# Performance work log

Hardware: AMD Instinct MI355X
Metric: run time of the kernel (lower is better)

Reference implementation:

```python
import jax, jax.numpy as jnp
import numpy as np
from jax import lax

D_MODEL = 1024
D_STATE = 16
EXPAND = 2
KERNEL = 4
BATCH = 4
SEQ = 4096
LN_EPS = 1e-5


def _ln(x, w, b):
    m = jnp.mean(x, axis=-1, keepdims=True)
    v = jnp.mean((x - m) ** 2, axis=-1, keepdims=True)
    return (x - m) * lax.rsqrt(v + LN_EPS) * w + b


def setup_inputs() -> dict:
    key = jax.random.key(0)
    ks = jax.random.split(key, 16)
    d, n, e, k = D_MODEL, D_STATE, EXPAND, KERNEL

    def lin(key, fan_in, shape):
        bound = 1.0 / np.sqrt(fan_in)
        return jax.random.uniform(key, shape, jnp.float32, -bound, bound)

    return {
        "x": jax.random.normal(ks[0], (BATCH, SEQ, d), jnp.float32),
        "ln1_w": jnp.ones((d,), jnp.float32),
        "ln1_b": jnp.zeros((d,), jnp.float32),
        "conv_w": lin(ks[1], k, (d, 1, k)),  # depthwise conv, groups=d -> fan_in=k
        "conv_b": lin(ks[2], k, (d,)),
        "lns_w": jnp.ones((d,), jnp.float32),
        "lns_b": jnp.zeros((d,), jnp.float32),
        "in_w": lin(ks[3], d, (d, 2 * d)),
        "in_b": lin(ks[4], d, (2 * d,)),
        "xp_w": lin(ks[5], d, (d, n)),
        "xp_b": lin(ks[6], d, (n,)),
        "A_log": jax.random.normal(ks[7], (n,), jnp.float32),
        "D": jax.random.normal(ks[8], (n, d), jnp.float32),
        "out_w": lin(ks[9], d, (d, d)),
        "out_b": lin(ks[10], d, (d,)),
        "ln2_w": jnp.ones((d,), jnp.float32),
        "ln2_b": jnp.zeros((d,), jnp.float32),
        "mlp_w1": lin(ks[11], d, (d, e * d)),
        "mlp_b1": lin(ks[12], d, (e * d,)),
        "mlp_w2": lin(ks[13], e * d, (e * d, d)),
        "mlp_b2": lin(ks[14], e * d, (d,)),
    }


def reference(x, ln1_w, ln1_b, conv_w, conv_b, lns_w, lns_b, in_w, in_b,
              xp_w, xp_b, A_log, D, out_w, out_b, ln2_w, ln2_b,
              mlp_w1, mlp_b1, mlp_w2, mlp_b2):
    b, s, d = x.shape
    # --- depthwise causal-padded conv branch (truncated to seq_len) ---
    xn = _ln(x, ln1_w, ln1_b)
    xc = jnp.transpose(xn, (0, 2, 1))  # (b, d, s)
    xc = lax.conv_general_dilated(
        xc, conv_w, window_strides=(1,), padding=[(KERNEL - 1, KERNEL - 1)],
        feature_group_count=d, dimension_numbers=("NCH", "OIH", "NCH"))
    xc = xc + conv_b[None, :, None]
    xc = jnp.transpose(xc, (0, 2, 1))[:, :s]  # (b, s, d)
    x = x + xc

    # --- SelectiveScanLayer ---
    residual = x
    xn = _ln(x, lns_w, lns_b)
    xz = xn @ in_w + in_b
    xp, z = jnp.split(xz, 2, axis=-1)
    xp = jax.nn.silu(xp)
    z = jax.nn.sigmoid(z)
    u = xp @ xp_w + xp_b  # (b, s, n)
    decay = jnp.exp(-jnp.exp(A_log))  # exp(A), A = -exp(A_log); (n,)

    u_t = jnp.transpose(u, (1, 0, 2))  # (s, b, n)

    def step(h, u_i):
        h = decay * h + u_i
        return h, h

    _, hs = lax.scan(step, jnp.zeros((b, D_STATE), x.dtype), u_t)  # (s, b, n)
    ys = jnp.einsum("sbn,nd->sbd", hs, D) * jnp.transpose(z, (1, 0, 2))
    ys = ys @ out_w + out_b  # (s, b, d)
    # faithful to original: torch stack gives (1,s,b,d), then .view(b,s,d)
    y = ys.reshape(b, s, d)
    x = residual + y

    # --- MLP (dropout inactive at eval) ---
    h = _ln(x, ln2_w, ln2_b)
    h = jax.nn.gelu(h @ mlp_w1 + mlp_b1, approximate=False)
    h = h @ mlp_w2 + mlp_b2
    return x + h
```

## Files before the change

kernel.cpp:

```cpp
#include <hip/hip_runtime.h>
#include <cstdint>
#include <cstddef>


typedef short bf16x8 __attribute__((ext_vector_type(8)));
typedef float f32x4 __attribute__((ext_vector_type(4)));

#define GLD16(gp, lp)                                                          \
  __builtin_amdgcn_global_load_lds(                                            \
      (__attribute__((address_space(1))) void*)(gp),                           \
      (__attribute__((address_space(3))) void*)(lp), 16, 0, 0)

static __device__ __forceinline__ ushort f2bf(float f) {
  union { float f; uint32_t u; } c; c.f = f;
  uint32_t r = c.u + 0x7FFFu + ((c.u >> 16) & 1u);
  return (ushort)(r >> 16);
}
static __device__ __forceinline__ float bf2f(ushort u) {
  union { uint32_t u; float f; } c; c.u = ((uint32_t)u) << 16;
  return c.f;
}

template <int BF16OUT>
__global__ __launch_bounds__(256) void ln_kernel(
    const float* __restrict__ x, const float* __restrict__ w,
    const float* __restrict__ b, void* __restrict__ out) {
  const int row = blockIdx.x;
  const int tid = threadIdx.x;
  const float4 v = ((const float4*)(x + (size_t)row * 1024))[tid];
  float s  = v.x + v.y + v.z + v.w;
  float s2 = v.x * v.x + v.y * v.y + v.z * v.z + v.w * v.w;
#pragma unroll
  for (int off = 32; off > 0; off >>= 1) {
    s  += __shfl_down(s, off);
    s2 += __shfl_down(s2, off);
  }
  __shared__ float red[8];
  const int wv = tid >> 6, ln = tid & 63;
  if (ln == 0) { red[wv] = s; red[4 + wv] = s2; }
  __syncthreads();
  s  = red[0] + red[1] + red[2] + red[3];
  s2 = red[4] + red[5] + red[6] + red[7];
  const float mean = s * (1.f / 1024.f);
  const float var  = s2 * (1.f / 1024.f) - mean * mean;
  const float rstd = rsqrtf(var + 1e-5f);
  const float4 wv4 = ((const float4*)w)[tid];
  const float4 bv4 = ((const float4*)b)[tid];
  const float o0 = (v.x - mean) * rstd * wv4.x + bv4.x;
  const float o1 = (v.y - mean) * rstd * wv4.y + bv4.y;
  const float o2 = (v.z - mean) * rstd * wv4.z + bv4.z;
  const float o3 = (v.w - mean) * rstd * wv4.w + bv4.w;
  if (BF16OUT) {
    ushort4 o; o.x = f2bf(o0); o.y = f2bf(o1); o.z = f2bf(o2); o.w = f2bf(o3);
    ((ushort4*)((ushort*)out + (size_t)row * 1024))[tid] = o;
  } else {
    float4 o; o.x = o0; o.y = o1; o.z = o2; o.w = o3;
    ((float4*)((float*)out + (size_t)row * 1024))[tid] = o;
  }
}

__global__ __launch_bounds__(256) void conv_kernel(
    const float* __restrict__ x, const float* __restrict__ xn,
    const float* __restrict__ cw, const float* __restrict__ cb,
    float* __restrict__ x1) {
  const size_t i = (size_t)blockIdx.x * 256 + threadIdx.x;
  const int c4 = (int)(i & 255);
  const size_t row = i >> 8;
  const int t = (int)(row & 4095);
  const int c0 = c4 * 4;
  float4 acc = *(const float4*)(cb + c0);
  const float4 w0 = *(const float4*)(cw + (size_t)(c0 + 0) * 4);
  const float4 w1 = *(const float4*)(cw + (size_t)(c0 + 1) * 4);
  const float4 w2 = *(const float4*)(cw + (size_t)(c0 + 2) * 4);
  const float4 w3 = *(const float4*)(cw + (size_t)(c0 + 3) * 4);
  const float4* xnb = (const float4*)xn;
  const size_t rowbase = (row - (size_t)t) << 8;
#pragma unroll
  for (int j = 0; j < 4; j++) {
    const int tt = t - 3 + j;
    if (tt >= 0) {
      const float4 xv = xnb[rowbase + (size_t)tt * 256 + c4];
      acc.x += xv.x * ((const float*)&w0)[j];
      acc.y += xv.y * ((const float*)&w1)[j];
      acc.z += xv.z * ((const float*)&w2)[j];
      acc.w += xv.w * ((const float*)&w3)[j];
    }
  }
  const float4 xv0 = ((const float4*)x)[i];
  float4 o;
  o.x = xv0.x + acc.x; o.y = xv0.y + acc.y;
  o.z = xv0.z + acc.z; o.w = xv0.w + acc.w;
  ((float4*)x1)[i] = o;
}

__global__ __launch_bounds__(256) void wt_kernel(
    const float* __restrict__ w, ushort* __restrict__ wt, int K, int N) {
  __shared__ float tile[32][33];
  const int tx = threadIdx.x & 31, ty = threadIdx.x >> 5;
  const int n0 = blockIdx.x * 32, k0 = blockIdx.y * 32;
#pragma unroll
  for (int j = 0; j < 32; j += 8)
    tile[ty + j][tx] = w[(size_t)(k0 + ty + j) * N + n0 + tx];
  __syncthreads();
#pragma unroll
  for (int j = 0; j < 32; j += 8)
    wt[(size_t)(n0 + ty + j) * K + k0 + tx] = f2bf(tile[tx][ty + j]);
}

__global__ __launch_bounds__(256) void u_kernel(
    const ushort* __restrict__ xp, const float* __restrict__ w,
    const float* __restrict__ wb, float* __restrict__ u) {
  const int tid = threadIdx.x;
  const int r = tid >> 4, n = tid & 15;
  const size_t row = (size_t)blockIdx.x * 16 + r;
  const ushort* xr = xp + row * 1024;
  float acc = wb[n];
  for (int k = 0; k < 1024; k += 8) {
    const uint4 pk = *(const uint4*)(xr + k);
    const ushort* pp = (const ushort*)&pk;
#pragma unroll
    for (int j = 0; j < 8; j++)
      acc += bf2f(pp[j]) * w[(size_t)(k + j) * 16 + n];
  }
  u[row * 16 + n] = acc;
}

__global__ __launch_bounds__(256) void scan_kernel(
    const float* __restrict__ u, const float* __restrict__ A_log,
    float* __restrict__ hs) {
  const int tid = threadIdx.x;
  const int b = blockIdx.x >> 4;
  const int n = blockIdx.x & 15;
  const float d = expf(-expf(A_log[n]));
  const int t0 = tid * 16;
  const float* up = u + ((size_t)b * 4096) * 16 + n;
  float loc[16];
  float h = 0.f;
#pragma unroll
  for (int i = 0; i < 16; i++) {
    h = d * h + up[(size_t)(t0 + i) * 16];
    loc[i] = h;
  }
  __shared__ float sv[256];
  sv[tid] = h;
  __syncthreads();
  float d16 = d * d; d16 *= d16; d16 *= d16; d16 *= d16;
  float f = d16;
  for (int off = 1; off < 256; off <<= 1) {
    const float add = (tid >= off) ? sv[tid - off] : 0.f;
    __syncthreads();
    sv[tid] += f * add;
    __syncthreads();
    f *= f;
  }
  const float carry = (tid > 0) ? sv[tid - 1] : 0.f;
  float dp = d;
#pragma unroll
  for (int i = 0; i < 16; i++) {
    const float hg = loc[i] + dp * carry;
    dp *= d;
    hs[((size_t)(t0 + i) * 4 + b) * 16 + n] = hg;
  }
}

__global__ __launch_bounds__(256) void g_kernel(
    const float* __restrict__ hs, const float* __restrict__ Dm,
    const ushort* __restrict__ z, ushort* __restrict__ g) {
  __shared__ float hsh[256];
  const int tid = threadIdx.x;
  const int r0 = blockIdx.x * 16;
  hsh[tid] = hs[(size_t)r0 * 16 + tid];
  __syncthreads();
  float4 acc[16];
#pragma unroll
  for (int rr = 0; rr < 16; rr++) acc[rr] = make_float4(0.f, 0.f, 0.f, 0.f);
  const float4* Dv = (const float4*)Dm;
#pragma unroll
  for (int n = 0; n < 16; n++) {
    const float4 dv = Dv[(size_t)n * 256 + tid];
#pragma unroll
    for (int rr = 0; rr < 16; rr++) {
      const float h = hsh[rr * 16 + n];
      acc[rr].x += h * dv.x; acc[rr].y += h * dv.y;
      acc[rr].z += h * dv.z; acc[rr].w += h * dv.w;
    }
  }
#pragma unroll
  for (int rr = 0; rr < 16; rr++) {
    const int r = r0 + rr;
    const int b = r & 3, t = r >> 2;
    const ushort4 zv =
        *(const ushort4*)(z + ((size_t)b * 4096 + t) * 1024 + tid * 4);
    ushort4 o;
    o.x = f2bf(acc[rr].x * bf2f(zv.x)); o.y = f2bf(acc[rr].y * bf2f(zv.y));
    o.z = f2bf(acc[rr].z * bf2f(zv.z)); o.w = f2bf(acc[rr].w * bf2f(zv.w));
    *(ushort4*)(g + (size_t)r * 1024 + tid * 4) = o;
  }
}

template <int EPI>
__global__ __launch_bounds__(256) void gemm_bt(
    const ushort* __restrict__ A, const ushort* __restrict__ Bt,
    const float* __restrict__ bias, int K, void* __restrict__ p0,
    void* __restrict__ p1) {
  __shared__ ushort As[128 * 32];
  __shared__ ushort Bs[128 * 32];
  const int tid = threadIdx.x;
  const int wave = tid >> 6, lane = tid & 63;
  const int l16 = lane & 15, quad = lane >> 4;
  const int bm0 = blockIdx.y * 128, bn0 = blockIdx.x * 128;
  const int wr = (wave >> 1) * 64, wc = (wave & 1) * 64;
  const int srow = lane >> 2;
  const int skel = (((lane & 3) ^ ((srow >> 1) & 3)) << 3);

  const ushort* Ag = A + (size_t)(bm0 + wave * 32 + srow) * K + skel;
  const ushort* Bg = Bt + (size_t)(bn0 + wave * 32 + srow) * K + skel;
  ushort* Al = &As[wave * 32 * 32];
  ushort* Bl = &Bs[wave * 32 * 32];

  const int rswz = (l16 >> 1) & 3;
  const int coff = ((quad ^ rswz) << 3);

  f32x4 acc[4][4];
#pragma unroll
  for (int i = 0; i < 4; i++)
#pragma unroll
    for (int j = 0; j < 4; j++) acc[i][j] = (f32x4){0.f, 0.f, 0.f, 0.f};

  for (int k0 = 0; k0 < K; k0 += 32) {
    GLD16(Ag + k0, Al);
    GLD16(Ag + k0 + (size_t)16 * K, Al + 16 * 32);
    GLD16(Bg + k0, Bl);
    GLD16(Bg + k0 + (size_t)16 * K, Bl + 16 * 32);
    __syncthreads();
    bf16x8 aF[4], bF[4];
#pragma unroll
    for (int i = 0; i < 4; i++)
      aF[i] = *(const bf16x8*)&As[(wr + i * 16 + l16) * 32 + coff];
#pragma unroll
    for (int j = 0; j < 4; j++)
      bF[j] = *(const bf16x8*)&Bs[(wc + j * 16 + l16) * 32 + coff];
#pragma unroll
    for (int i = 0; i < 4; i++)
#pragma unroll
      for (int j = 0; j < 4; j++)
        acc[i][j] = __builtin_amdgcn_mfma_f32_16x16x32_bf16(
            aF[i], bF[j], acc[i][j], 0, 0, 0);
    __syncthreads();
  }

#pragma unroll
  for (int i = 0; i < 4; i++) {
    const int row0 = bm0 + wr + i * 16 + quad * 4;
#pragma unroll
    for (int j = 0; j < 4; j++) {
      const int c = bn0 + wc + j * 16 + l16;
      const float bv = bias[c];
#pragma unroll
      for (int r = 0; r < 4; r++) {
        const size_t row = (size_t)(row0 + r);
        const float v = acc[i][j][r] + bv;
        if (EPI == 0) {
          if (c < 1024)
            ((ushort*)p0)[row * 1024 + c] = f2bf(v / (1.f + __expf(-v)));
          else
            ((ushort*)p1)[row * 1024 + (c - 1024)] =
                f2bf(1.f / (1.f + __expf(-v)));
        } else if (EPI == 1) {
          float* io = (float*)p0;
          io[row * 1024 + c] += v;
        } else if (EPI == 2) {
          ((ushort*)p0)[row * 2048 + c] =
              f2bf(0.5f * v * (1.f + erff(v * 0.70710678118654752f)));
        } else {
          ((float*)p0)[row * 1024 + c] =
              ((const float*)p1)[row * 1024 + c] + v;
        }
      }
    }
  }
}

extern "C" void kernel_launch(void* const* d_in, const int* in_sizes, int n_in,
                              void* d_out, int out_size, void* d_ws,
                              size_t ws_size, hipStream_t stream) {
  const float* x      = (const float*)d_in[0];
  const float* ln1_w  = (const float*)d_in[1];
  const float* ln1_b  = (const float*)d_in[2];
  const float* conv_w = (const float*)d_in[3];
  const float* conv_b = (const float*)d_in[4];
  const float* lns_w  = (const float*)d_in[5];
  const float* lns_b  = (const float*)d_in[6];
  const float* in_w   = (const float*)d_in[7];
  const float* in_b   = (const float*)d_in[8];
  const float* xp_w   = (const float*)d_in[9];
  const float* xp_b   = (const float*)d_in[10];
  const float* A_log  = (const float*)d_in[11];
  const float* Dm     = (const float*)d_in[12];
  const float* out_w  = (const float*)d_in[13];
  const float* out_b  = (const float*)d_in[14];
  const float* ln2_w  = (const float*)d_in[15];
  const float* ln2_b  = (const float*)d_in[16];
  const float* mlp_w1 = (const float*)d_in[17];
  const float* mlp_b1 = (const float*)d_in[18];
  const float* mlp_w2 = (const float*)d_in[19];
  const float* mlp_b2 = (const float*)d_in[20];

  char* wsp = (char*)d_ws;
  size_t off = 0;
  auto alloc = [&](size_t bytes) {
    void* p = wsp + off;
    off += (bytes + 255) & ~(size_t)255;
    return p;
  };
  float*  x1    = (float*)alloc(67108864);
  float*  xn    = (float*)alloc(67108864);
  ushort* abuf  = (ushort*)xn;
  ushort* gbuf  = (ushort*)xn + 16777216;
  ushort* xpb   = (ushort*)alloc(33554432);
  ushort* zb    = (ushort*)alloc(67108864);
  ushort* h1b   = (ushort*)zb;
  float*  ub    = (float*)alloc(1048576);
  float*  hsb   = (float*)alloc(1048576);
  ushort* in_wT = (ushort*)alloc(4194304);
  ushort* out_wT= (ushort*)alloc(2097152);
  ushort* w1T   = (ushort*)alloc(4194304);
  ushort* w2T   = (ushort*)alloc(4194304);

  wt_kernel<<<dim3(64, 32), 256, 0, stream>>>(in_w, in_wT, 1024, 2048);
  wt_kernel<<<dim3(32, 32), 256, 0, stream>>>(out_w, out_wT, 1024, 1024);
  wt_kernel<<<dim3(64, 32), 256, 0, stream>>>(mlp_w1, w1T, 1024, 2048);
  wt_kernel<<<dim3(32, 64), 256, 0, stream>>>(mlp_w2, w2T, 2048, 1024);

  ln_kernel<0><<<16384, 256, 0, stream>>>(x, ln1_w, ln1_b, xn);
  conv_kernel<<<16384, 256, 0, stream>>>(x, xn, conv_w, conv_b, x1);
  ln_kernel<1><<<16384, 256, 0, stream>>>(x1, lns_w, lns_b, abuf);
  gemm_bt<0><<<dim3(16, 128), 256, 0, stream>>>(abuf, in_wT, in_b, 1024,
                                                xpb, zb);
  u_kernel<<<1024, 256, 0, stream>>>(xpb, xp_w, xp_b, ub);
  scan_kernel<<<64, 256, 0, stream>>>(ub, A_log, hsb);
  g_kernel<<<1024, 256, 0, stream>>>(hsb, Dm, zb, gbuf);
  gemm_bt<1><<<dim3(8, 128), 256, 0, stream>>>(gbuf, out_wT, out_b, 1024,
                                               x1, nullptr);
  ln_kernel<1><<<16384, 256, 0, stream>>>(x1, ln2_w, ln2_b, xpb);
  gemm_bt<2><<<dim3(16, 128), 256, 0, stream>>>(xpb, w1T, mlp_b1, 1024,
                                                h1b, nullptr);
  gemm_bt<3><<<dim3(8, 128), 256, 0, stream>>>(h1b, w2T, mlp_b2, 2048,
                                               d_out, x1);
}
```

Measured before the change: 767.2 us.

## Fuse LN+conv+LN, merge weight transposes, MFMA u-projection, deeper GEMM K-tile

Fuses the first layernorm, depthwise conv, residual add and second layernorm into one kernel that recomputes the LN of the 3 preceding rows instead of writing and rereading an fp32 normalized buffer. Merges the four weight-transpose launches into one. Replaces the scalar u projection with an MFMA kernel that stages bf16 weights in LDS. The main GEMM's K-step grows from 32 to 64 with a new XOR swizzle, and the grid swaps x/y so consecutive blocks walk M. These cut memory traffic and launch count, at the cost of redundant LN reductions in the fused kernel and more LDS per GEMM block.

```diff
diff --git a/kernel.cpp b/kernel.cpp
--- a/kernel.cpp
+++ b/kernel.cpp
@@ -59,70 +59,174 @@
   }
 }
 
-__global__ __launch_bounds__(256) void conv_kernel(
-    const float* __restrict__ x, const float* __restrict__ xn,
-    const float* __restrict__ cw, const float* __restrict__ cb,
-    float* __restrict__ x1) {
-  const size_t i = (size_t)blockIdx.x * 256 + threadIdx.x;
-  const int c4 = (int)(i & 255);
-  const size_t row = i >> 8;
-  const int t = (int)(row & 4095);
-  const int c0 = c4 * 4;
+__global__ __launch_bounds__(256) void lnconv_kernel(
+    const float* __restrict__ x, const float* __restrict__ ln1w,
+    const float* __restrict__ ln1b, const float* __restrict__ cw,
+    const float* __restrict__ cb, const float* __restrict__ lnsw,
+    const float* __restrict__ lnsb, float* __restrict__ x1,
+    ushort* __restrict__ abuf) {
+  const int row = blockIdx.x;
+  const int t = row & 4095;
+  const int tid = threadIdx.x;
+  const int wv = tid >> 6, ln = tid & 63;
+  const float4* x4 = (const float4*)x;
+  float4 xr[4];
+  float s[4], q[4];
+#pragma unroll
+  for (int j = 0; j < 4; j++) {
+    const int tt = t - 3 + j;
+    if (tt >= 0)
+      xr[j] = x4[(size_t)(row - 3 + j) * 256 + tid];
+    else
+      xr[j] = make_float4(0.f, 0.f, 0.f, 0.f);
+    s[j] = xr[j].x + xr[j].y + xr[j].z + xr[j].w;
+    q[j] = xr[j].x * xr[j].x + xr[j].y * xr[j].y + xr[j].z * xr[j].z +
+           xr[j].w * xr[j].w;
+  }
+#pragma unroll
+  for (int off = 32; off > 0; off >>= 1) {
+#pragma unroll
+    for (int j = 0; j < 4; j++) {
+      s[j] += __shfl_down(s[j], off);
+      q[j] += __shfl_down(q[j], off);
+    }
+  }
+  __shared__ float red[4][8];
+  __shared__ float red2[8];
+  if (ln == 0) {
+#pragma unroll
+    for (int j = 0; j < 4; j++) { red[wv][j] = s[j]; red[wv][4 + j] = q[j]; }
+  }
+  __syncthreads();
+  float4 wv4 = ((const float4*)ln1w)[tid];
+  float4 bv4 = ((const float4*)ln1b)[tid];
+  const int c0 = tid * 4;
   float4 acc = *(const float4*)(cb + c0);
   const float4 w0 = *(const float4*)(cw + (size_t)(c0 + 0) * 4);
   const float4 w1 = *(const float4*)(cw + (size_t)(c0 + 1) * 4);
   const float4 w2 = *(const float4*)(cw + (size_t)(c0 + 2) * 4);
   const float4 w3 = *(const float4*)(cw + (size_t)(c0 + 3) * 4);
-  const float4* xnb = (const float4*)xn;
-  const size_t rowbase = (row - (size_t)t) << 8;
 #pragma unroll
   for (int j = 0; j < 4; j++) {
-    const int tt = t - 3 + j;
-    if (tt >= 0) {
-      const float4 xv = xnb[rowbase + (size_t)tt * 256 + c4];
-      acc.x += xv.x * ((const float*)&w0)[j];
-      acc.y += xv.y * ((const float*)&w1)[j];
-      acc.z += xv.z * ((const float*)&w2)[j];
-      acc.w += xv.w * ((const float*)&w3)[j];
-    }
-  }
-  const float4 xv0 = ((const float4*)x)[i];
+    if (t - 3 + j >= 0) {
+      const float sm = red[0][j] + red[1][j] + red[2][j] + red[3][j];
+      const float sq = red[0][4 + j] + red[1][4 + j] + red[2][4 + j] +
+                       red[3][4 + j];
+      const float mean = sm * (1.f / 1024.f);
+      const float var  = sq * (1.f / 1024.f) - mean * mean;
+      const float rstd = rsqrtf(var + 1e-5f);
+      const float lx = (xr[j].x - mean) * rstd * wv4.x + bv4.x;
+      const float ly = (xr[j].y - mean) * rstd * wv4.y + bv4.y;
+      const float lz = (xr[j].z - mean) * rstd * wv4.z + bv4.z;
+      const float lw = (xr[j].w - mean) * rstd * wv4.w + bv4.w;
+      acc.x += lx * ((const float*)&w0)[j];
+      acc.y += ly * ((const float*)&w1)[j];
+      acc.z += lz * ((const float*)&w2)[j];
+      acc.w += lw * ((const float*)&w3)[j];
+    }
+  }
   float4 o;
-  o.x = xv0.x + acc.x; o.y = xv0.y + acc.y;
-  o.z = xv0.z + acc.z; o.w = xv0.w + acc.w;
-  ((float4*)x1)[i] = o;
-}
-
-__global__ __launch_bounds__(256) void wt_kernel(
-    const float* __restrict__ w, ushort* __restrict__ wt, int K, int N) {
+  o.x = xr[3].x + acc.x; o.y = xr[3].y + acc.y;
+  o.z = xr[3].z + acc.z; o.w = xr[3].w + acc.w;
+  ((float4*)x1)[(size_t)row * 256 + tid] = o;
+  float s2 = o.x + o.y + o.z + o.w;
+  float q2 = o.x * o.x + o.y * o.y + o.z * o.z + o.w * o.w;
+#pragma unroll
+  for (int off = 32; off > 0; off >>= 1) {
+    s2 += __shfl_down(s2, off);
+    q2 += __shfl_down(q2, off);
+  }
+  if (ln == 0) { red2[wv] = s2; red2[4 + wv] = q2; }
+  __syncthreads();
+  const float sm = red2[0] + red2[1] + red2[2] + red2[3];
+  const float sq = red2[4] + red2[5] + red2[6] + red2[7];
+  const float mean = sm * (1.f / 1024.f);
+  const float var  = sq * (1.f / 1024.f) - mean * mean;
+  const float rstd = rsqrtf(var + 1e-5f);
+  wv4 = ((const float4*)lnsw)[tid];
+  bv4 = ((const float4*)lnsb)[tid];
+  ushort4 a;
+  a.x = f2bf((o.x - mean) * rstd * wv4.x + bv4.x);
+  a.y = f2bf((o.y - mean) * rstd * wv4.y + bv4.y);
+  a.z = f2bf((o.z - mean) * rstd * wv4.z + bv4.z);
+  a.w = f2bf((o.w - mean) * rstd * wv4.w + bv4.w);
+  ((ushort4*)(abuf + (size_t)row * 1024))[tid] = a;
+}
+
+__global__ __launch_bounds__(256) void wt_all_kernel(
+    const float* __restrict__ in_w, const float* __restrict__ out_w,
+    const float* __restrict__ w1, const float* __restrict__ w2,
+    ushort* __restrict__ in_wT, ushort* __restrict__ out_wT,
+    ushort* __restrict__ w1T, ushort* __restrict__ w2T) {
   __shared__ float tile[32][33];
+  const int idx = blockIdx.x;
+  const float* src; ushort* dst; int K, N, n0, k0;
+  if (idx < 2048) {
+    src = in_w; dst = in_wT; K = 1024; N = 2048;
+    n0 = (idx & 63) * 32; k0 = (idx >> 6) * 32;
+  } else if (idx < 3072) {
+    const int r = idx - 2048;
+    src = out_w; dst = out_wT; K = 1024; N = 1024;
+    n0 = (r & 31) * 32; k0 = (r >> 5) * 32;
+  } else if (idx < 5120) {
+    const int r = idx - 3072;
+    src = w1; dst = w1T; K = 1024; N = 2048;
+    n0 = (r & 63) * 32; k0 = (r >> 6) * 32;
+  } else {
+    const int r = idx - 5120;
+    src = w2; dst = w2T; K = 2048; N = 1024;
+    n0 = (r & 31) * 32; k0 = (r >> 5) * 32;
+  }
   const int tx = threadIdx.x & 31, ty = threadIdx.x >> 5;
-  const int n0 = blockIdx.x * 32, k0 = blockIdx.y * 32;
 #pragma unroll
   for (int j = 0; j < 32; j += 8)
-    tile[ty + j][tx] = w[(size_t)(k0 + ty + j) * N + n0 + tx];
+    tile[ty + j][tx] = src[(size_t)(k0 + ty + j) * N + n0 + tx];
   __syncthreads();
 #pragma unroll
   for (int j = 0; j < 32; j += 8)
-    wt[(size_t)(n0 + ty + j) * K + k0 + tx] = f2bf(tile[tx][ty + j]);
-}
-
-__global__ __launch_bounds__(256) void u_kernel(
-    const ushort* __restrict__ xp, const float* __restrict__ w,
-    const float* __restrict__ wb, float* __restrict__ u) {
-  const int tid = threadIdx.x;
-  const int r = tid >> 4, n = tid & 15;
-  const size_t row = (size_t)blockIdx.x * 16 + r;
-  const ushort* xr = xp + row * 1024;
-  float acc = wb[n];
-  for (int k = 0; k < 1024; k += 8) {
-    const uint4 pk = *(const uint4*)(xr + k);
-    const ushort* pp = (const ushort*)&pk;
-#pragma unroll
-    for (int j = 0; j < 8; j++)
-      acc += bf2f(pp[j]) * w[(size_t)(k + j) * 16 + n];
-  }
-  u[row * 16 + n] = acc;
+    dst[(size_t)(n0 + ty + j) * K + k0 + tx] = f2bf(tile[tx][ty + j]);
+}
+
+__global__ __launch_bounds__(256) void u_mfma_kernel(
+    const ushort* __restrict__ xp, const float* __restrict__ xpw,
+    const float* __restrict__ xpb, float* __restrict__ u) {
+  __shared__ ushort Ws[16 * 1024];
+  __shared__ ushort As[64 * 64];
+  const int tid = threadIdx.x;
+  const int wave = tid >> 6, lane = tid & 63;
+  const int l16 = lane & 15, quad = lane >> 4;
+  for (int e = tid; e < 16384; e += 256) {
+    const int n = e & 15, k = e >> 4;
+    Ws[n * 1024 + (((k >> 3) ^ (n & 7)) << 3) + (k & 7)] =
+        f2bf(xpw[(size_t)k * 16 + n]);
+  }
+  const int bm0 = blockIdx.x * 64;
+  const int srow = lane >> 3, sblk = (lane & 7) ^ (srow & 7);
+  const ushort* Ag = xp + (size_t)(bm0 + wave * 16 + srow) * 1024 + sblk * 8;
+  ushort* Al = &As[wave * 16 * 64];
+  const int rsw = l16 & 7;
+  f32x4 acc = (f32x4){0.f, 0.f, 0.f, 0.f};
+  __syncthreads();
+  for (int k0 = 0; k0 < 1024; k0 += 64) {
+    GLD16(Ag + k0, Al);
+    GLD16(Ag + k0 + (size_t)8 * 1024, Al + 512);
+    __syncthreads();
+#pragma unroll
+    for (int kh = 0; kh < 2; kh++) {
+      const bf16x8 aF = *(const bf16x8*)
+          &As[(wave * 16 + l16) * 64 + (((kh * 4 + quad) ^ rsw) << 3)];
+      const bf16x8 bF = *(const bf16x8*)
+          &Ws[l16 * 1024 + ((((k0 >> 3) + kh * 4 + quad) ^ rsw) << 3)];
+      acc = __builtin_amdgcn_mfma_f32_16x16x32_bf16(aF, bF, acc, 0, 0, 0);
+    }
+    __syncthreads();
+  }
+  const float bv = xpb[l16];
+#pragma unroll
+  for (int r = 0; r < 4; r++) {
+    const int row = bm0 + wave * 16 + quad * 4 + r;
+    u[(size_t)row * 16 + l16] = acc[r] + bv;
+  }
 }
 
 __global__ __launch_bounds__(256) void scan_kernel(
@@ -203,23 +307,21 @@
     const ushort* __restrict__ A, const ushort* __restrict__ Bt,
     const float* __restrict__ bias, int K, void* __restrict__ p0,
     void* __restrict__ p1) {
-  __shared__ ushort As[128 * 32];
-  __shared__ ushort Bs[128 * 32];
+  __shared__ ushort As[128 * 64];
+  __shared__ ushort Bs[128 * 64];
   const int tid = threadIdx.x;
   const int wave = tid >> 6, lane = tid & 63;
   const int l16 = lane & 15, quad = lane >> 4;
-  const int bm0 = blockIdx.y * 128, bn0 = blockIdx.x * 128;
+  const int bm0 = blockIdx.x * 128, bn0 = blockIdx.y * 128;
   const int wr = (wave >> 1) * 64, wc = (wave & 1) * 64;
-  const int srow = lane >> 2;
-  const int skel = (((lane & 3) ^ ((srow >> 1) & 3)) << 3);
-
-  const ushort* Ag = A + (size_t)(bm0 + wave * 32 + srow) * K + skel;
-  const ushort* Bg = Bt + (size_t)(bn0 + wave * 32 + srow) * K + skel;
-  ushort* Al = &As[wave * 32 * 32];
-  ushort* Bl = &Bs[wave * 32 * 32];
-
-  const int rswz = (l16 >> 1) & 3;
-  const int coff = ((quad ^ rswz) << 3);
+  const int srow = lane >> 3;
+  const int sblk = (lane & 7) ^ (srow & 7);
+
+  const ushort* Ag = A + (size_t)(bm0 + wave * 32 + srow) * K + sblk * 8;
+  const ushort* Bg = Bt + (size_t)(bn0 + wave * 32 + srow) * K + sblk * 8;
+  ushort* Al = &As[wave * 32 * 64];
+  ushort* Bl = &Bs[wave * 32 * 64];
+  const int rsw = l16 & 7;
 
   f32x4 acc[4][4];
 #pragma unroll
@@ -227,25 +329,30 @@
 #pragma unroll
     for (int j = 0; j < 4; j++) acc[i][j] = (f32x4){0.f, 0.f, 0.f, 0.f};
 
-  for (int k0 = 0; k0 < K; k0 += 32) {
-    GLD16(Ag + k0, Al);
-    GLD16(Ag + k0 + (size_t)16 * K, Al + 16 * 32);
-    GLD16(Bg + k0, Bl);
-    GLD16(Bg + k0 + (size_t)16 * K, Bl + 16 * 32);
-    __syncthreads();
-    bf16x8 aF[4], bF[4];
-#pragma unroll
-    for (int i = 0; i < 4; i++)
-      aF[i] = *(const bf16x8*)&As[(wr + i * 16 + l16) * 32 + coff];
-#pragma unroll
-    for (int j = 0; j < 4; j++)
-      bF[j] = *(const bf16x8*)&Bs[(wc + j * 16 + l16) * 32 + coff];
-#pragma unroll
-    for (int i = 0; i < 4; i++)
+  for (int k0 = 0; k0 < K; k0 += 64) {
+#pragma unroll
+    for (int i = 0; i < 4; i++) {
+      GLD16(Ag + (size_t)(i * 8) * K + k0, Al + i * 512);
+      GLD16(Bg + (size_t)(i * 8) * K + k0, Bl + i * 512);
+    }
+    __syncthreads();
+#pragma unroll
+    for (int kh = 0; kh < 2; kh++) {
+      const int c8 = ((kh * 4 + quad) ^ rsw) << 3;
+      bf16x8 aF[4], bF[4];
+#pragma unroll
+      for (int i = 0; i < 4; i++)
+        aF[i] = *(const bf16x8*)&As[(wr + i * 16 + l16) * 64 + c8];
 #pragma unroll
       for (int j = 0; j < 4; j++)
-        acc[i][j] = __builtin_amdgcn_mfma_f32_16x16x32_bf16(
-            aF[i], bF[j], acc[i][j], 0, 0, 0);
+        bF[j] = *(const bf16x8*)&Bs[(wc + j * 16 + l16) * 64 + c8];
+#pragma unroll
+      for (int i = 0; i < 4; i++)
+#pragma unroll
+        for (int j = 0; j < 4; j++)
+          acc[i][j] = __builtin_amdgcn_mfma_f32_16x16x32_bf16(
+              aF[i], bF[j], acc[i][j], 0, 0, 0);
+    }
     __syncthreads();
   }
 
@@ -314,9 +421,8 @@
     return p;
   };
   float*  x1    = (float*)alloc(67108864);
-  float*  xn    = (float*)alloc(67108864);
-  ushort* abuf  = (ushort*)xn;
-  ushort* gbuf  = (ushort*)xn + 16777216;
+  ushort* abuf  = (ushort*)alloc(67108864);
+  ushort* gbuf  = abuf + 16777216;
   ushort* xpb   = (ushort*)alloc(33554432);
   ushort* zb    = (ushort*)alloc(67108864);
   ushort* h1b   = (ushort*)zb;
@@ -327,24 +433,20 @@
   ushort* w1T   = (ushort*)alloc(4194304);
   ushort* w2T   = (ushort*)alloc(4194304);
 
-  wt_kernel<<<dim3(64, 32), 256, 0, stream>>>(in_w, in_wT, 1024, 2048);
-  wt_kernel<<<dim3(32, 32), 256, 0, stream>>>(out_w, out_wT, 1024, 1024);
-  wt_kernel<<<dim3(64, 32), 256, 0, stream>>>(mlp_w1, w1T, 1024, 2048);
-  wt_kernel<<<dim3(32, 64), 256, 0, stream>>>(mlp_w2, w2T, 2048, 1024);
-
-  ln_kernel<0><<<16384, 256, 0, stream>>>(x, ln1_w, ln1_b, xn);
-  conv_kernel<<<16384, 256, 0, stream>>>(x, xn, conv_w, conv_b, x1);
-  ln_kernel<1><<<16384, 256, 0, stream>>>(x1, lns_w, lns_b, abuf);
-  gemm_bt<0><<<dim3(16, 128), 256, 0, stream>>>(abuf, in_wT, in_b, 1024,
+  wt_all_kernel<<<7168, 256, 0, stream>>>(in_w, out_w, mlp_w1, mlp_w2,
+                                          in_wT, out_wT, w1T, w2T);
+  lnconv_kernel<<<16384, 256, 0, stream>>>(x, ln1_w, ln1_b, conv_w, conv_b,
+                                           lns_w, lns_b, x1, abuf);
+  gemm_bt<0><<<dim3(128, 16), 256, 0, stream>>>(abuf, in_wT, in_b, 1024,
                                                 xpb, zb);
-  u_kernel<<<1024, 256, 0, stream>>>(xpb, xp_w, xp_b, ub);
+  u_mfma_kernel<<<256, 256, 0, stream>>>(xpb, xp_w, xp_b, ub);
   scan_kernel<<<64, 256, 0, stream>>>(ub, A_log, hsb);
   g_kernel<<<1024, 256, 0, stream>>>(hsb, Dm, zb, gbuf);
-  gemm_bt<1><<<dim3(8, 128), 256, 0, stream>>>(gbuf, out_wT, out_b, 1024,
+  gemm_bt<1><<<dim3(128, 8), 256, 0, stream>>>(gbuf, out_wT, out_b, 1024,
                                                x1, nullptr);
   ln_kernel<1><<<16384, 256, 0, stream>>>(x1, ln2_w, ln2_b, xpb);
-  gemm_bt<2><<<dim3(16, 128), 256, 0, stream>>>(xpb, w1T, mlp_b1, 1024,
+  gemm_bt<2><<<dim3(128, 16), 256, 0, stream>>>(xpb, w1T, mlp_b1, 1024,
                                                 h1b, nullptr);
-  gemm_bt<3><<<dim3(8, 128), 256, 0, stream>>>(h1b, w2T, mlp_b2, 2048,
+  gemm_bt<3><<<dim3(128, 8), 256, 0, stream>>>(h1b, w2T, mlp_b2, 2048,
                                                d_out, x1);
 }
```

After: 688.7 us. 1.11x faster.
